# Performance work log

Measured on AMD Instinct MI355X. Metric: run time of the kernel, lower is better.

Reference implementation:

```python
import jax, jax.numpy as jnp
import numpy as np

# --- problem dims (see shape_source) ---
B, N0, N1 = 8, 50000, 12500        # batch, fine mesh verts, coarse mesh verts
E = 400000                          # graph edges (avg degree 8)
FIN, C, K, Z = 3, 32, 6, 128        # in feats, conv width, Chebyshev order, latent
DOWN_NNZ = N1 * 4                   # 4 fine verts pooled per coarse vert
UP_NNZ = N0 * 3                     # barycentric upsampling, 3 coarse verts per fine vert


def setup_inputs() -> dict:
    rng = np.random.default_rng(0)
    x = rng.standard_normal((B, N0, FIN)).astype(np.float32)

    # adjacency edges + symmetric-normalized Chebyshev norm (as ChebConv_batch.norm)
    src = rng.integers(0, N0, E)
    dst = rng.integers(0, N0, E)
    edge_index = np.stack([src, dst]).astype(np.int32)
    deg = np.bincount(src, minlength=N0).astype(np.float32)
    dinv = np.where(deg > 0, deg ** -0.5, 0.0).astype(np.float32)
    A_norm = (-dinv[src] * dinv[dst]).astype(np.float32)

    # sparse pooling matrices (row=output vert, col=input vert, val=weight)
    down_row = np.repeat(np.arange(N1), 4)
    down_col = rng.integers(0, N0, DOWN_NNZ)
    down_val = (rng.random(DOWN_NNZ) * 0.25).astype(np.float32)
    up_row = np.repeat(np.arange(N0), 3)
    up_col = rng.integers(0, N1, UP_NNZ)
    up_val = (rng.random(UP_NNZ) / 3.0).astype(np.float32)

    def w(*shape):
        return jnp.asarray((rng.standard_normal(shape) * 0.1).astype(np.float32))

    return {
        "x": jnp.asarray(x),
        "edge_index": jnp.asarray(edge_index),
        "A_norm": jnp.asarray(A_norm),
        "down_idx": jnp.asarray(np.stack([down_row, down_col]).astype(np.int32)),
        "down_val": jnp.asarray(down_val),
        "up_idx": jnp.asarray(np.stack([up_row, up_col]).astype(np.int32)),
        "up_val": jnp.asarray(up_val),
        "W_enc0": w(K, FIN, C), "b_enc0": w(C),
        "W_dec0": w(K, C, C), "b_dec0": w(C),
        "W_dec1": w(K, C, FIN),                      # final conv: bias=None
        "enc_lin_W": w(N1 * C, Z), "enc_lin_b": w(Z),
        "dec_lin_W": w(Z, N1 * C), "dec_lin_b": w(N1 * C),
    }


def _propagate(y, src, dst, norm):
    # y: [B, N, C]; out[:, i] = sum_{e: dst[e]==i} norm[e] * y[:, src[e]]
    m = y[:, src, :] * norm[None, :, None]          # [B, E, C] gather + scale
    return jnp.zeros_like(y).at[:, dst, :].add(m)   # scatter-add


def cheb_conv(x, edge_index, norm, W, b):
    # x: [B, N, Cin]; W: [K, Cin, Cout]; Chebyshev recursion T_k(L~) x
    src, dst = edge_index[0], edge_index[1]
    Tx0 = x
    out = jnp.einsum('bnc,co->bno', Tx0, W[0])
    if W.shape[0] > 1:
        Tx1 = _propagate(x, src, dst, norm)
        out = out + jnp.einsum('bnc,co->bno', Tx1, W[1])
    for k in range(2, W.shape[0]):
        Tx2 = 2.0 * _propagate(Tx1, src, dst, norm) - Tx0
        out = out + jnp.einsum('bnc,co->bno', Tx2, W[k])
        Tx0, Tx1 = Tx1, Tx2
    if b is not None:
        out = out + b
    return out


def surface_pool(x, row, col, val, n_out):
    # out = P @ x per batch, P sparse [n_out, n_in] with (row, col, val)
    m = x[:, col, :] * val[None, :, None]           # [B, nnz, C]
    out = jnp.zeros((x.shape[0], n_out, x.shape[2]), x.dtype)
    return out.at[:, row, :].add(m)


def reference(x, edge_index, A_norm, down_idx, down_val, up_idx, up_val,
              W_enc0, b_enc0, W_dec0, b_dec0, W_dec1,
              enc_lin_W, enc_lin_b, dec_lin_W, dec_lin_b):
    # encoder
    h = jax.nn.relu(cheb_conv(x, edge_index, A_norm, W_enc0, b_enc0))
    h = surface_pool(h, down_idx[0], down_idx[1], down_val, N1)
    z = h.reshape(B, N1 * C) @ enc_lin_W + enc_lin_b
    # decoder
    h = jax.nn.relu(z @ dec_lin_W + dec_lin_b).reshape(B, N1, C)
    h = surface_pool(h, up_idx[0], up_idx[1], up_val, N0)
    h = jax.nn.relu(cheb_conv(h, edge_index, A_norm, W_dec0, b_dec0))
    recon = cheb_conv(h, edge_index, A_norm, W_dec1, None)  # last layer: no bias
    return recon
```

## Files before the change

kernel.cpp:

```cpp
#include <hip/hip_runtime.h>

constexpr int B   = 8;
constexpr int N0  = 50000;
constexpr int N1  = 12500;
constexpr int E   = 400000;
constexpr int FIN = 3;
constexpr int C   = 32;
constexpr int Z   = 128;
constexpr int M   = N1 * C;
constexpr int DOWN_NNZ = N1 * 4;
constexpr int UP_NNZ   = N0 * 3;
constexpr size_t BN4 = (size_t)B * N0 * 4;

__global__ void k_hist(const int* __restrict__ dst, int* __restrict__ cnt) {
    int e = blockIdx.x * 256 + threadIdx.x;
    if (e < E) atomicAdd(&cnt[dst[e]], 1);
}

__global__ void k_scan_chunk(const int* __restrict__ cnt, int* __restrict__ rp,
                             int* __restrict__ part) {
    __shared__ int s[512];
    int t = threadIdx.x;
    int i = blockIdx.x * 512 + t;
    int v = (i < N0) ? cnt[i] : 0;
    s[t] = v;
    __syncthreads();
    for (int off = 1; off < 512; off <<= 1) {
        int add = (t >= off) ? s[t - off] : 0;
        __syncthreads();
        s[t] += add;
        __syncthreads();
    }
    if (i < N0) rp[i] = s[t] - v;
    if (t == 511) part[blockIdx.x] = s[511];
}

__global__ void k_scan_part(int* part, int nb) {
    if (threadIdx.x == 0 && blockIdx.x == 0) {
        int run = 0;
        for (int c = 0; c < nb; c++) { int t = part[c]; part[c] = run; run += t; }
    }
}

__global__ void k_scan_add(const int* __restrict__ part, int* __restrict__ rp,
                           int* __restrict__ pos) {
    int i = blockIdx.x * 256 + threadIdx.x;
    if (i < N0) {
        int r = rp[i] + part[i >> 9];
        rp[i] = r; pos[i] = r;
        if (i == 0) rp[N0] = E;
    }
}

__global__ void k_scatter(const int* __restrict__ ei, const float* __restrict__ norm,
                          int* __restrict__ pos, int* __restrict__ col_s,
                          float* __restrict__ val_s) {
    int e = blockIdx.x * 256 + threadIdx.x;
    if (e < E) {
        int d = ei[E + e];
        int j = atomicAdd(&pos[d], 1);
        col_s[j] = ei[e];
        val_s[j] = norm[e];
    }
}

template <int SSTR, int USTR, int OSTR, bool HAS_G, bool HAS_SUB, bool SCALE2>
__global__ void k_prop3g(const int* __restrict__ rp, const int* __restrict__ col,
                         const float* __restrict__ val, const float* __restrict__ src,
                         const float* __restrict__ g, const float* __restrict__ sub,
                         float* __restrict__ out) {
    int bid = blockIdx.x;
    int b = bid & 7;
    int n = (bid >> 3) * 256 + threadIdx.x;
    if (n >= N0) return;
    const float* sb = src + (size_t)b * N0 * SSTR;
    int s = rp[n], e = rp[n + 1];
    float x0[8], x1[8], x2[8];
#pragma unroll
    for (int u = 0; u < 8; u++) { x0[u] = 0.f; x1[u] = 0.f; x2[u] = 0.f; }
    for (int base = s; base < e; base += 8) {
        int jc[8]; float wv[8];
#pragma unroll
        for (int u = 0; u < 8; u++) {
            int jj = base + u;
            bool p = jj < e;
            int ji = p ? jj : s;
            jc[u] = col[ji];
            wv[u] = p ? val[ji] : 0.f;
        }
#pragma unroll
        for (int u = 0; u < 8; u++) {
            if (SSTR == 4) {
                float4 v = *(const float4*)(sb + (size_t)jc[u] * 4);
                x0[u] += wv[u] * v.x; x1[u] += wv[u] * v.y; x2[u] += wv[u] * v.z;
            } else {
                const float* p = sb + (size_t)jc[u] * 3;
                x0[u] += wv[u] * p[0]; x1[u] += wv[u] * p[1]; x2[u] += wv[u] * p[2];
            }
        }
    }
    float a0 = ((x0[0] + x0[1]) + (x0[2] + x0[3])) + ((x0[4] + x0[5]) + (x0[6] + x0[7]));
    float a1 = ((x1[0] + x1[1]) + (x1[2] + x1[3])) + ((x1[4] + x1[5]) + (x1[6] + x1[7]));
    float a2 = ((x2[0] + x2[1]) + (x2[2] + x2[3])) + ((x2[4] + x2[5]) + (x2[6] + x2[7]));
    if (SCALE2) { a0 *= 2.f; a1 *= 2.f; a2 *= 2.f; }
    if (HAS_G) {
        const float* gp = g + ((size_t)b * N0 + n) * 4;
        a0 += gp[0]; a1 += gp[1]; a2 += gp[2];
    }
    if (HAS_SUB) {
        const float* up = sub + ((size_t)b * N0 + n) * USTR;
        a0 -= up[0]; a1 -= up[1]; a2 -= up[2];
    }
    if (OSTR == 4) {
        *(float4*)(out + ((size_t)b * N0 + n) * 4) = make_float4(a0, a1, a2, 0.f);
    } else {
        float* op = out + ((size_t)b * N0 + n) * 3;
        op[0] = a0; op[1] = a1; op[2] = a2;
    }
}

__global__ void k_enc_combine(const float* __restrict__ x,
                              const float* __restrict__ T1, const float* __restrict__ T2,
                              const float* __restrict__ T3, const float* __restrict__ T4,
                              const float* __restrict__ T5,
                              const float* __restrict__ W, const float* __restrict__ bias,
                              float* __restrict__ out) {
    int o = threadIdx.x & 31, nl = threadIdx.x >> 5;
    int n = blockIdx.x * 8 + nl;
    int b = blockIdx.y;
    size_t b3 = ((size_t)b * N0 + n) * 3;
    size_t b4 = ((size_t)b * N0 + n) * 4;
    float t[18];
    t[0] = x[b3 + 0]; t[1] = x[b3 + 1]; t[2] = x[b3 + 2];
    const float* Ts[5] = { T1, T2, T3, T4, T5 };
#pragma unroll
    for (int k = 0; k < 5; k++) {
        t[3 + k * 3 + 0] = Ts[k][b4 + 0];
        t[3 + k * 3 + 1] = Ts[k][b4 + 1];
        t[3 + k * 3 + 2] = Ts[k][b4 + 2];
    }
    float acc = bias[o];
#pragma unroll
    for (int q = 0; q < 18; q++) acc += t[q] * W[q * 32 + o];
    out[((size_t)b * N0 + n) * 32 + o] = fmaxf(acc, 0.f);
}

__global__ void k_pool4(const int* __restrict__ dcol, const float* __restrict__ dval,
                        const float* __restrict__ src, float* __restrict__ out) {
    int bid = blockIdx.x;
    int b = bid & 7;
    int c = threadIdx.x & 31, rl = threadIdx.x >> 5;
    int r = (bid >> 3) * 8 + rl;
    if (r >= N1) return;
    const float* sb = src + (size_t)b * N0 * 32;
    float a = 0.f;
#pragma unroll
    for (int t = 0; t < 4; t++) {
        int idx = 4 * r + t;
        a += dval[idx] * sb[(size_t)dcol[idx] * 32 + c];
    }
    out[((size_t)b * N1 + r) * 32 + c] = a;
}

__global__ void k_pool3_init(const int* __restrict__ ucol, const float* __restrict__ uval,
                             const float* __restrict__ src, const float* __restrict__ W,
                             const float* __restrict__ bias,
                             float* __restrict__ hup, float* __restrict__ acc) {
    int bid = blockIdx.x;
    int b = bid & 7;
    int c = threadIdx.x & 31, rl = threadIdx.x >> 5;
    int i = (bid >> 3) * 8 + rl;
    const float* sb = src + (size_t)b * N1 * 32;
    float a = 0.f;
#pragma unroll
    for (int t = 0; t < 3; t++) {
        int idx = 3 * i + t;
        a += uval[idx] * sb[(size_t)ucol[idx] * 32 + c];
    }
    size_t base = ((size_t)b * N0 + i) * 32;
    hup[base + c] = a;
    float Wr[32];
#pragma unroll
    for (int cc = 0; cc < 32; cc++) Wr[cc] = W[cc * 32 + c];
    float o0 = bias[c], o1 = 0.f, o2 = 0.f, o3 = 0.f;
#pragma unroll
    for (int cc = 0; cc < 32; cc += 4) {
        o0 += __shfl(a, cc, 32) * Wr[cc];
        o1 += __shfl(a, cc + 1, 32) * Wr[cc + 1];
        o2 += __shfl(a, cc + 2, 32) * Wr[cc + 2];
        o3 += __shfl(a, cc + 3, 32) * Wr[cc + 3];
    }
    acc[base + c] = (o0 + o1) + (o2 + o3);
}

__global__ void k_enclin1(const float* __restrict__ S0, const float* __restrict__ W,
                          float* __restrict__ partial) {
    int zl = threadIdx.x & 127, half = threadIdx.x >> 7;
    int m0 = blockIdx.x * 128;
    float acc[B];
#pragma unroll
    for (int b = 0; b < B; b++) acc[b] = 0.f;
    for (int i = 0; i < 64; i++) {
        int m = m0 + half + 2 * i;
        float w = W[(size_t)m * Z + zl];
#pragma unroll
        for (int b = 0; b < B; b++) acc[b] += S0[(size_t)b * M + m] * w;
    }
    __shared__ float red[128 * B];
    if (half == 1) {
#pragma unroll
        for (int b = 0; b < B; b++) red[zl * B + b] = acc[b];
    }
    __syncthreads();
    if (half == 0) {
#pragma unroll
        for (int b = 0; b < B; b++)
            partial[(size_t)blockIdx.x * 1024 + b * 128 + zl] = acc[b] + red[zl * B + b];
    }
}

__global__ void k_enclin2a(const float* __restrict__ partial, float* __restrict__ p2) {
    int i  = blockIdx.x * 256 + threadIdx.x;
    int kc = blockIdx.y;
    int k0 = kc * 125;
    float a = 0.f;
    for (int k = k0; k < k0 + 125; k++) a += partial[(size_t)k * 1024 + i];
    p2[(size_t)kc * 1024 + i] = a;
}

__global__ void k_enclin2b(const float* __restrict__ p2, const float* __restrict__ bias,
                           float* __restrict__ z) {
    int i = blockIdx.x * 256 + threadIdx.x;
    if (i >= B * Z) return;
    float a = bias[i & 127];
#pragma unroll
    for (int k = 0; k < 25; k++) a += p2[(size_t)k * 1024 + i];
    z[i] = a;
}

__global__ void k_declin(const float* __restrict__ z, const float* __restrict__ W,
                         const float* __restrict__ bias, float* __restrict__ out) {
    __shared__ float zs[B * Z];
    for (int i = threadIdx.x; i < B * Z; i += 256) zs[i] = z[i];
    __syncthreads();
    int m = blockIdx.x * 256 + threadIdx.x;
    if (m >= M) return;
    float bv = bias[m];
    float acc[B];
#pragma unroll
    for (int b = 0; b < B; b++) acc[b] = bv;
    for (int j = 0; j < Z; j++) {
        float w = W[(size_t)j * M + m];
#pragma unroll
        for (int b = 0; b < B; b++) acc[b] += zs[b * Z + j] * w;
    }
#pragma unroll
    for (int b = 0; b < B; b++) out[(size_t)b * M + m] = fmaxf(acc[b], 0.f);
}

template <bool HAS_SUB, bool WRITE_TX>
__global__ void k_prop_fused32(const int* __restrict__ rp, const int* __restrict__ col,
                               const float* __restrict__ val, const float* __restrict__ src,
                               const float* __restrict__ sub, float* __restrict__ txout,
                               const float* __restrict__ W, float* __restrict__ accb) {
    int bid = blockIdx.x;
    int b = bid & 7;
    int lane = threadIdx.x & 31, nl = threadIdx.x >> 5;
    int n = (bid >> 3) * 8 + nl;
    int s = rp[n], e = rp[n + 1];
    const float* sb = src + (size_t)b * N0 * 32;
    float acc[8];
#pragma unroll
    for (int u = 0; u < 8; u++) acc[u] = 0.f;
    for (int base = s; base < e; base += 8) {
        int jc[8]; float wv[8];
#pragma unroll
        for (int u = 0; u < 8; u++) {
            int jj = base + u;
            bool p = jj < e;
            int ji = p ? jj : s;
            jc[u] = col[ji];
            wv[u] = p ? val[ji] : 0.f;
        }
#pragma unroll
        for (int u = 0; u < 8; u++)
            acc[u] += wv[u] * sb[(size_t)jc[u] * 32 + lane];
    }
    float a = ((acc[0] + acc[1]) + (acc[2] + acc[3])) + ((acc[4] + acc[5]) + (acc[6] + acc[7]));
    float Wr[32];
#pragma unroll
    for (int cc = 0; cc < 32; cc++) Wr[cc] = W[cc * 32 + lane];
    size_t base2 = ((size_t)b * N0 + n) * 32;
    float t = HAS_SUB ? 2.f * a - sub[base2 + lane] : a;
    if (WRITE_TX) txout[base2 + lane] = t;
    float o0 = 0.f, o1 = 0.f, o2 = 0.f, o3 = 0.f;
#pragma unroll
    for (int cc = 0; cc < 32; cc += 4) {
        o0 += __shfl(t, cc, 32) * Wr[cc];
        o1 += __shfl(t, cc + 1, 32) * Wr[cc + 1];
        o2 += __shfl(t, cc + 2, 32) * Wr[cc + 2];
        o3 += __shfl(t, cc + 3, 32) * Wr[cc + 3];
    }
    accb[base2 + lane] += (o0 + o1) + (o2 + o3);
}

__global__ void k_proj(const float* __restrict__ ACC, const float* __restrict__ W1,
                       float* __restrict__ G) {
    int lane = threadIdx.x & 31, nl = threadIdx.x >> 5;
    int n = blockIdx.x * 8 + nl;
    int k = (lane < 18) ? lane / 3 : 0;
    int c = (lane < 18) ? lane % 3 : 0;
    float Wr[32];
#pragma unroll
    for (int cc = 0; cc < 32; cc++) Wr[cc] = W1[k * 96 + cc * 3 + c];
#pragma unroll
    for (int b = 0; b < B; b++) {
        float t = fmaxf(ACC[((size_t)b * N0 + n) * 32 + lane], 0.f);
        float o0 = 0.f, o1 = 0.f, o2 = 0.f, o3 = 0.f;
#pragma unroll
        for (int cc = 0; cc < 32; cc += 4) {
            o0 += __shfl(t, cc, 32) * Wr[cc];
            o1 += __shfl(t, cc + 1, 32) * Wr[cc + 1];
            o2 += __shfl(t, cc + 2, 32) * Wr[cc + 2];
            o3 += __shfl(t, cc + 3, 32) * Wr[cc + 3];
        }
        if (lane < 18)
            G[(size_t)k * BN4 + ((size_t)b * N0 + n) * 4 + c] = (o0 + o1) + (o2 + o3);
    }
}

extern "C" void kernel_launch(void* const* d_in, const int* in_sizes, int n_in,
                              void* d_out, int out_size, void* d_ws, size_t ws_size,
                              hipStream_t stream) {
    const float* x        = (const float*)d_in[0];
    const int*   ei       = (const int*)d_in[1];
    const float* A_norm   = (const float*)d_in[2];
    const int*   down_idx = (const int*)d_in[3];
    const float* down_val = (const float*)d_in[4];
    const int*   up_idx   = (const int*)d_in[5];
    const float* up_val   = (const float*)d_in[6];
    const float* W_enc0   = (const float*)d_in[7];
    const float* b_enc0   = (const float*)d_in[8];
    const float* W_dec0   = (const float*)d_in[9];
    const float* b_dec0   = (const float*)d_in[10];
    const float* W_dec1   = (const float*)d_in[11];
    const float* enc_lin_W = (const float*)d_in[12];
    const float* enc_lin_b = (const float*)d_in[13];
    const float* dec_lin_W = (const float*)d_in[14];
    const float* dec_lin_b = (const float*)d_in[15];
    float* OUT = (float*)d_out;

    char* w8 = (char*)d_ws;
    auto alignup = [](size_t v) { return (v + 255) & ~(size_t)255; };
    size_t off = 0;
    auto carve = [&](size_t bytes) { void* p = w8 + off; off = alignup(off + bytes); return p; };

    int*   row_ptr = (int*)carve((size_t)(N0 + 1) * 4);
    int*   poscnt  = (int*)carve((size_t)N0 * 4);
    int*   part    = (int*)carve(128 * 4);
    int*   col_s   = (int*)carve((size_t)E * 4 + 64);
    float* val_s   = (float*)carve((size_t)E * 4 + 64);
    float* zbuf    = (float*)carve((size_t)B * Z * 4);
    constexpr size_t BIG = (size_t)B * N0 * C;
    float* A1 = (float*)carve(BIG * 4);
    float* A2 = (float*)carve(BIG * 4);
    float* A3 = (float*)carve(BIG * 4);
    (void)ws_size; (void)n_in; (void)in_sizes; (void)out_size;

    float* T1 = A1 + 0 * BN4;
    float* T2 = A1 + 1 * BN4;
    float* T3 = A1 + 2 * BN4;
    float* T4 = A1 + 3 * BN4;
    float* T5 = A1 + 4 * BN4;
    float* HENC = A2;
    float* S0   = A3;
    float* PART = A2;
    float* P2   = A3 + (size_t)8 * 1024 * 1024;
    float* S1   = A1;
    float* HUP  = A2;
    float* ACC  = A3;
    float* G    = A1;
    float* B4   = A2 + 0 * BN4;
    float* B3   = A2 + 1 * BN4;
    float* B2   = A2 + 2 * BN4;
    float* B1   = A2 + 3 * BN4;

    const int* dcol = down_idx + DOWN_NNZ;
    const int* ucol = up_idx + UP_NNZ;

    dim3 blk(256);
    dim3 gE((E + 255) / 256);
    dim3 gN0t((N0 + 255) / 256);
    dim3 g3x(((N0 + 255) / 256) * 8);
    dim3 gN8(N0 / 8);
    dim3 gNB(N0 / 8, B);
    dim3 gF(N0);
    dim3 gP4(((N1 + 7) / 8) * 8);

    hipMemsetAsync(poscnt, 0, (size_t)N0 * 4, stream);
    k_hist<<<gE, blk, 0, stream>>>(ei + E, poscnt);
    int nchunks = (N0 + 511) / 512;
    k_scan_chunk<<<nchunks, 512, 0, stream>>>(poscnt, row_ptr, part);
    k_scan_part<<<1, 1, 0, stream>>>(part, nchunks);
    k_scan_add<<<gN0t, blk, 0, stream>>>(part, row_ptr, poscnt);
    k_scatter<<<gE, blk, 0, stream>>>(ei, A_norm, poscnt, col_s, val_s);

    k_prop3g<3,3,4,false,false,false><<<g3x, blk, 0, stream>>>(row_ptr, col_s, val_s, x,  nullptr, nullptr, T1);
    k_prop3g<4,3,4,false,true, true ><<<g3x, blk, 0, stream>>>(row_ptr, col_s, val_s, T1, nullptr, x,  T2);
    k_prop3g<4,4,4,false,true, true ><<<g3x, blk, 0, stream>>>(row_ptr, col_s, val_s, T2, nullptr, T1, T3);
    k_prop3g<4,4,4,false,true, true ><<<g3x, blk, 0, stream>>>(row_ptr, col_s, val_s, T3, nullptr, T2, T4);
    k_prop3g<4,4,4,false,true, true ><<<g3x, blk, 0, stream>>>(row_ptr, col_s, val_s, T4, nullptr, T3, T5);
    k_enc_combine<<<gNB, blk, 0, stream>>>(x, T1, T2, T3, T4, T5, W_enc0, b_enc0, HENC);

    k_pool4<<<gP4, blk, 0, stream>>>(dcol, down_val, HENC, S0);

    k_enclin1<<<3125, blk, 0, stream>>>(S0, enc_lin_W, PART);
    dim3 g2a(4, 25);
    k_enclin2a<<<g2a, blk, 0, stream>>>(PART, P2);
    k_enclin2b<<<4, blk, 0, stream>>>(P2, enc_lin_b, zbuf);

    k_declin<<<(M + 255) / 256, blk, 0, stream>>>(zbuf, dec_lin_W, dec_lin_b, S1);

    k_pool3_init<<<gF, blk, 0, stream>>>(ucol, up_val, S1, W_dec0, b_dec0, HUP, ACC);

    k_prop_fused32<false, true ><<<gF, blk, 0, stream>>>(row_ptr, col_s, val_s, A2, nullptr, A1, W_dec0 + 1 * C * C, ACC);
    k_prop_fused32<true,  true ><<<gF, blk, 0, stream>>>(row_ptr, col_s, val_s, A1, A2, A2, W_dec0 + 2 * C * C, ACC);
    k_prop_fused32<true,  true ><<<gF, blk, 0, stream>>>(row_ptr, col_s, val_s, A2, A1, A1, W_dec0 + 3 * C * C, ACC);
    k_prop_fused32<true,  true ><<<gF, blk, 0, stream>>>(row_ptr, col_s, val_s, A1, A2, A2, W_dec0 + 4 * C * C, ACC);
    k_prop_fused32<true,  false><<<gF, blk, 0, stream>>>(row_ptr, col_s, val_s, A2, A1, nullptr, W_dec0 + 5 * C * C, ACC);

    k_proj<<<gN8, blk, 0, stream>>>(ACC, W_dec1, G);
    float* G0 = G + 0 * BN4; float* G1 = G + 1 * BN4; float* G2 = G + 2 * BN4;
    float* G3c = G + 3 * BN4; float* G4 = G + 4 * BN4; float* G5 = G + 5 * BN4;
    k_prop3g<4,4,4,true,false,true ><<<g3x, blk, 0, stream>>>(row_ptr, col_s, val_s, G5, G4, nullptr, B4);
    k_prop3g<4,4,4,true,true, true ><<<g3x, blk, 0, stream>>>(row_ptr, col_s, val_s, B4, G3c, G5, B3);
    k_prop3g<4,4,4,true,true, true ><<<g3x, blk, 0, stream>>>(row_ptr, col_s, val_s, B3, G2, B4, B2);
    k_prop3g<4,4,4,true,true, true ><<<g3x, blk, 0, stream>>>(row_ptr, col_s, val_s, B2, G1, B3, B1);
    k_prop3g<4,4,3,true,true, false><<<g3x, blk, 0, stream>>>(row_ptr, col_s, val_s, B1, G0, B2, OUT);
}
```

Before: 1.636 ms.

## Share CSR edge reads across batches in sparse propagation kernels

The 3-channel propagation kernel now handles two batch elements per thread, and the 32-channel fused propagation kernel handles all 8 batch elements per warp row. Each loaded column index and weight is reused across several batches, which cuts redundant CSR reads and the number of blocks launched. In exchange, register pressure rises (8-batch accumulators plus 32 weight registers) and there is less parallelism per launch, which may lower occupancy. The unroll over edges also drops from 8 to 4 or 2.

```diff
diff --git a/kernel.cpp b/kernel.cpp
--- a/kernel.cpp
+++ b/kernel.cpp
@@ -70,18 +70,22 @@
                          const float* __restrict__ g, const float* __restrict__ sub,
                          float* __restrict__ out) {
     int bid = blockIdx.x;
-    int b = bid & 7;
-    int n = (bid >> 3) * 256 + threadIdx.x;
+    int q = bid & 3;
+    int b0 = 2 * q, b1 = 2 * q + 1;
+    int n = (bid >> 2) * 256 + threadIdx.x;
     if (n >= N0) return;
-    const float* sb = src + (size_t)b * N0 * SSTR;
+    const float* s0 = src + (size_t)b0 * N0 * SSTR;
+    const float* s1 = src + (size_t)b1 * N0 * SSTR;
     int s = rp[n], e = rp[n + 1];
-    float x0[8], x1[8], x2[8];
-#pragma unroll
-    for (int u = 0; u < 8; u++) { x0[u] = 0.f; x1[u] = 0.f; x2[u] = 0.f; }
-    for (int base = s; base < e; base += 8) {
-        int jc[8]; float wv[8];
-#pragma unroll
-        for (int u = 0; u < 8; u++) {
+    float xa[4][3], xb[4][3];
+#pragma unroll
+    for (int u = 0; u < 4; u++)
+#pragma unroll
+        for (int c = 0; c < 3; c++) { xa[u][c] = 0.f; xb[u][c] = 0.f; }
+    for (int base = s; base < e; base += 4) {
+        int jc[4]; float wv[4];
+#pragma unroll
+        for (int u = 0; u < 4; u++) {
             int jj = base + u;
             bool p = jj < e;
             int ji = p ? jj : s;
@@ -89,33 +93,42 @@
             wv[u] = p ? val[ji] : 0.f;
         }
 #pragma unroll
-        for (int u = 0; u < 8; u++) {
+        for (int u = 0; u < 4; u++) {
             if (SSTR == 4) {
-                float4 v = *(const float4*)(sb + (size_t)jc[u] * 4);
-                x0[u] += wv[u] * v.x; x1[u] += wv[u] * v.y; x2[u] += wv[u] * v.z;
+                float4 va = *(const float4*)(s0 + (size_t)jc[u] * 4);
+                float4 vb = *(const float4*)(s1 + (size_t)jc[u] * 4);
+                xa[u][0] += wv[u] * va.x; xa[u][1] += wv[u] * va.y; xa[u][2] += wv[u] * va.z;
+                xb[u][0] += wv[u] * vb.x; xb[u][1] += wv[u] * vb.y; xb[u][2] += wv[u] * vb.z;
             } else {
-                const float* p = sb + (size_t)jc[u] * 3;
-                x0[u] += wv[u] * p[0]; x1[u] += wv[u] * p[1]; x2[u] += wv[u] * p[2];
+                const float* pa = s0 + (size_t)jc[u] * 3;
+                const float* pb = s1 + (size_t)jc[u] * 3;
+                xa[u][0] += wv[u] * pa[0]; xa[u][1] += wv[u] * pa[1]; xa[u][2] += wv[u] * pa[2];
+                xb[u][0] += wv[u] * pb[0]; xb[u][1] += wv[u] * pb[1]; xb[u][2] += wv[u] * pb[2];
             }
         }
     }
-    float a0 = ((x0[0] + x0[1]) + (x0[2] + x0[3])) + ((x0[4] + x0[5]) + (x0[6] + x0[7]));
-    float a1 = ((x1[0] + x1[1]) + (x1[2] + x1[3])) + ((x1[4] + x1[5]) + (x1[6] + x1[7]));
-    float a2 = ((x2[0] + x2[1]) + (x2[2] + x2[3])) + ((x2[4] + x2[5]) + (x2[6] + x2[7]));
-    if (SCALE2) { a0 *= 2.f; a1 *= 2.f; a2 *= 2.f; }
-    if (HAS_G) {
-        const float* gp = g + ((size_t)b * N0 + n) * 4;
-        a0 += gp[0]; a1 += gp[1]; a2 += gp[2];
-    }
-    if (HAS_SUB) {
-        const float* up = sub + ((size_t)b * N0 + n) * USTR;
-        a0 -= up[0]; a1 -= up[1]; a2 -= up[2];
-    }
-    if (OSTR == 4) {
-        *(float4*)(out + ((size_t)b * N0 + n) * 4) = make_float4(a0, a1, a2, 0.f);
-    } else {
-        float* op = out + ((size_t)b * N0 + n) * 3;
-        op[0] = a0; op[1] = a1; op[2] = a2;
+#pragma unroll
+    for (int half = 0; half < 2; half++) {
+        int b = half ? b1 : b0;
+        float (*x)[3] = half ? xb : xa;
+        float a0 = (x[0][0] + x[1][0]) + (x[2][0] + x[3][0]);
+        float a1 = (x[0][1] + x[1][1]) + (x[2][1] + x[3][1]);
+        float a2 = (x[0][2] + x[1][2]) + (x[2][2] + x[3][2]);
+        if (SCALE2) { a0 *= 2.f; a1 *= 2.f; a2 *= 2.f; }
+        if (HAS_G) {
+            const float* gp = g + ((size_t)b * N0 + n) * 4;
+            a0 += gp[0]; a1 += gp[1]; a2 += gp[2];
+        }
+        if (HAS_SUB) {
+            const float* up = sub + ((size_t)b * N0 + n) * USTR;
+            a0 -= up[0]; a1 -= up[1]; a2 -= up[2];
+        }
+        if (OSTR == 4) {
+            *(float4*)(out + ((size_t)b * N0 + n) * 4) = make_float4(a0, a1, a2, 0.f);
+        } else {
+            float* op = out + ((size_t)b * N0 + n) * 3;
+            op[0] = a0; op[1] = a1; op[2] = a2;
+        }
     }
 }
 
@@ -263,45 +276,46 @@
                                const float* __restrict__ val, const float* __restrict__ src,
                                const float* __restrict__ sub, float* __restrict__ txout,
                                const float* __restrict__ W, float* __restrict__ accb) {
-    int bid = blockIdx.x;
-    int b = bid & 7;
     int lane = threadIdx.x & 31, nl = threadIdx.x >> 5;
-    int n = (bid >> 3) * 8 + nl;
+    int n = blockIdx.x * 8 + nl;
     int s = rp[n], e = rp[n + 1];
-    const float* sb = src + (size_t)b * N0 * 32;
-    float acc[8];
-#pragma unroll
-    for (int u = 0; u < 8; u++) acc[u] = 0.f;
-    for (int base = s; base < e; base += 8) {
-        int jc[8]; float wv[8];
-#pragma unroll
-        for (int u = 0; u < 8; u++) {
-            int jj = base + u;
-            bool p = jj < e;
-            int ji = p ? jj : s;
-            jc[u] = col[ji];
-            wv[u] = p ? val[ji] : 0.f;
-        }
-#pragma unroll
-        for (int u = 0; u < 8; u++)
-            acc[u] += wv[u] * sb[(size_t)jc[u] * 32 + lane];
-    }
-    float a = ((acc[0] + acc[1]) + (acc[2] + acc[3])) + ((acc[4] + acc[5]) + (acc[6] + acc[7]));
+    float accA[B], accB2[B];
+#pragma unroll
+    for (int b = 0; b < B; b++) { accA[b] = 0.f; accB2[b] = 0.f; }
+    for (int base = s; base < e; base += 2) {
+        bool p1 = base + 1 < e;
+        int c0 = col[base];
+        int c1 = col[p1 ? base + 1 : base];
+        float w0 = val[base];
+        float w1 = p1 ? val[base + 1] : 0.f;
+        size_t o0 = (size_t)c0 * 32 + lane;
+        size_t o1 = (size_t)c1 * 32 + lane;
+#pragma unroll
+        for (int b = 0; b < B; b++) {
+            const float* sb = src + (size_t)b * (N0 * 32);
+            accA[b]  += w0 * sb[o0];
+            accB2[b] += w1 * sb[o1];
+        }
+    }
     float Wr[32];
 #pragma unroll
     for (int cc = 0; cc < 32; cc++) Wr[cc] = W[cc * 32 + lane];
-    size_t base2 = ((size_t)b * N0 + n) * 32;
-    float t = HAS_SUB ? 2.f * a - sub[base2 + lane] : a;
-    if (WRITE_TX) txout[base2 + lane] = t;
-    float o0 = 0.f, o1 = 0.f, o2 = 0.f, o3 = 0.f;
-#pragma unroll
-    for (int cc = 0; cc < 32; cc += 4) {
-        o0 += __shfl(t, cc, 32) * Wr[cc];
-        o1 += __shfl(t, cc + 1, 32) * Wr[cc + 1];
-        o2 += __shfl(t, cc + 2, 32) * Wr[cc + 2];
-        o3 += __shfl(t, cc + 3, 32) * Wr[cc + 3];
-    }
-    accb[base2 + lane] += (o0 + o1) + (o2 + o3);
+#pragma unroll
+    for (int b = 0; b < B; b++) {
+        float a = accA[b] + accB2[b];
+        size_t base2 = ((size_t)b * N0 + n) * 32;
+        float t = HAS_SUB ? 2.f * a - sub[base2 + lane] : a;
+        if (WRITE_TX) txout[base2 + lane] = t;
+        float o0 = 0.f, o1 = 0.f, o2 = 0.f, o3 = 0.f;
+#pragma unroll
+        for (int cc = 0; cc < 32; cc += 4) {
+            o0 += __shfl(t, cc, 32) * Wr[cc];
+            o1 += __shfl(t, cc + 1, 32) * Wr[cc + 1];
+            o2 += __shfl(t, cc + 2, 32) * Wr[cc + 2];
+            o3 += __shfl(t, cc + 3, 32) * Wr[cc + 3];
+        }
+        accb[base2 + lane] += (o0 + o1) + (o2 + o3);
+    }
 }
 
 __global__ void k_proj(const float* __restrict__ ACC, const float* __restrict__ W1,
@@ -391,7 +405,7 @@
     dim3 blk(256);
     dim3 gE((E + 255) / 256);
     dim3 gN0t((N0 + 255) / 256);
-    dim3 g3x(((N0 + 255) / 256) * 8);
+    dim3 g3p(((N0 + 255) / 256) * 4);
     dim3 gN8(N0 / 8);
     dim3 gNB(N0 / 8, B);
     dim3 gF(N0);
@@ -405,11 +419,11 @@
     k_scan_add<<<gN0t, blk, 0, stream>>>(part, row_ptr, poscnt);
     k_scatter<<<gE, blk, 0, stream>>>(ei, A_norm, poscnt, col_s, val_s);
 
-    k_prop3g<3,3,4,false,false,false><<<g3x, blk, 0, stream>>>(row_ptr, col_s, val_s, x,  nullptr, nullptr, T1);
-    k_prop3g<4,3,4,false,true, true ><<<g3x, blk, 0, stream>>>(row_ptr, col_s, val_s, T1, nullptr, x,  T2);
-    k_prop3g<4,4,4,false,true, true ><<<g3x, blk, 0, stream>>>(row_ptr, col_s, val_s, T2, nullptr, T1, T3);
-    k_prop3g<4,4,4,false,true, true ><<<g3x, blk, 0, stream>>>(row_ptr, col_s, val_s, T3, nullptr, T2, T4);
-    k_prop3g<4,4,4,false,true, true ><<<g3x, blk, 0, stream>>>(row_ptr, col_s, val_s, T4, nullptr, T3, T5);
+    k_prop3g<3,3,4,false,false,false><<<g3p, blk, 0, stream>>>(row_ptr, col_s, val_s, x,  nullptr, nullptr, T1);
+    k_prop3g<4,3,4,false,true, true ><<<g3p, blk, 0, stream>>>(row_ptr, col_s, val_s, T1, nullptr, x,  T2);
+    k_prop3g<4,4,4,false,true, true ><<<g3p, blk, 0, stream>>>(row_ptr, col_s, val_s, T2, nullptr, T1, T3);
+    k_prop3g<4,4,4,false,true, true ><<<g3p, blk, 0, stream>>>(row_ptr, col_s, val_s, T3, nullptr, T2, T4);
+    k_prop3g<4,4,4,false,true, true ><<<g3p, blk, 0, stream>>>(row_ptr, col_s, val_s, T4, nullptr, T3, T5);
     k_enc_combine<<<gNB, blk, 0, stream>>>(x, T1, T2, T3, T4, T5, W_enc0, b_enc0, HENC);
 
     k_pool4<<<gP4, blk, 0, stream>>>(dcol, down_val, HENC, S0);
@@ -423,18 +437,18 @@
 
     k_pool3_init<<<gF, blk, 0, stream>>>(ucol, up_val, S1, W_dec0, b_dec0, HUP, ACC);
 
-    k_prop_fused32<false, true ><<<gF, blk, 0, stream>>>(row_ptr, col_s, val_s, A2, nullptr, A1, W_dec0 + 1 * C * C, ACC);
-    k_prop_fused32<true,  true ><<<gF, blk, 0, stream>>>(row_ptr, col_s, val_s, A1, A2, A2, W_dec0 + 2 * C * C, ACC);
-    k_prop_fused32<true,  true ><<<gF, blk, 0, stream>>>(row_ptr, col_s, val_s, A2, A1, A1, W_dec0 + 3 * C * C, ACC);
-    k_prop_fused32<true,  true ><<<gF, blk, 0, stream>>>(row_ptr, col_s, val_s, A1, A2, A2, W_dec0 + 4 * C * C, ACC);
-    k_prop_fused32<true,  false><<<gF, blk, 0, stream>>>(row_ptr, col_s, val_s, A2, A1, nullptr, W_dec0 + 5 * C * C, ACC);
+    k_prop_fused32<false, true ><<<gN8, blk, 0, stream>>>(row_ptr, col_s, val_s, A2, nullptr, A1, W_dec0 + 1 * C * C, ACC);
+    k_prop_fused32<true,  true ><<<gN8, blk, 0, stream>>>(row_ptr, col_s, val_s, A1, A2, A2, W_dec0 + 2 * C * C, ACC);
+    k_prop_fused32<true,  true ><<<gN8, blk, 0, stream>>>(row_ptr, col_s, val_s, A2, A1, A1, W_dec0 + 3 * C * C, ACC);
+    k_prop_fused32<true,  true ><<<gN8, blk, 0, stream>>>(row_ptr, col_s, val_s, A1, A2, A2, W_dec0 + 4 * C * C, ACC);
+    k_prop_fused32<true,  false><<<gN8, blk, 0, stream>>>(row_ptr, col_s, val_s, A2, A1, nullptr, W_dec0 + 5 * C * C, ACC);
 
     k_proj<<<gN8, blk, 0, stream>>>(ACC, W_dec1, G);
     float* G0 = G + 0 * BN4; float* G1 = G + 1 * BN4; float* G2 = G + 2 * BN4;
     float* G3c = G + 3 * BN4; float* G4 = G + 4 * BN4; float* G5 = G + 5 * BN4;
-    k_prop3g<4,4,4,true,false,true ><<<g3x, blk, 0, stream>>>(row_ptr, col_s, val_s, G5, G4, nullptr, B4);
-    k_prop3g<4,4,4,true,true, true ><<<g3x, blk, 0, stream>>>(row_ptr, col_s, val_s, B4, G3c, G5, B3);
-    k_prop3g<4,4,4,true,true, true ><<<g3x, blk, 0, stream>>>(row_ptr, col_s, val_s, B3, G2, B4, B2);
-    k_prop3g<4,4,4,true,true, true ><<<g3x, blk, 0, stream>>>(row_ptr, col_s, val_s, B2, G1, B3, B1);
-    k_prop3g<4,4,3,true,true, false><<<g3x, blk, 0, stream>>>(row_ptr, col_s, val_s, B1, G0, B2, OUT);
-}
+    k_prop3g<4,4,4,true,false,true ><<<g3p, blk, 0, stream>>>(row_ptr, col_s, val_s, G5, G4, nullptr, B4);
+    k_prop3g<4,4,4,true,true, true ><<<g3p, blk, 0, stream>>>(row_ptr, col_s, val_s, B4, G3c, G5, B3);
+    k_prop3g<4,4,4,true,true, true ><<<g3p, blk, 0, stream>>>(row_ptr, col_s, val_s, B3, G2, B4, B2);
+    k_prop3g<4,4,4,true,true, true ><<<g3p, blk, 0, stream>>>(row_ptr, col_s, val_s, B2, G1, B3, B1);
+    k_prop3g<4,4,3,true,true, false><<<g3p, blk, 0, stream>>>(row_ptr, col_s, val_s, B1, G0, B2, OUT);
+}
```

After: 1.478 ms. -9.7%, faster.
